# Performance work log

Measured on AMD Instinct MI355X. Metric: run time of the kernel, lower is better.

The kernel has to match this reference:

```python
import jax, jax.numpy as jnp
import numpy as np

VOCAB = 50257
EMBED = 256
OUT = 5
B = 512
S = 512

def setup_inputs() -> dict:
    key = jax.random.key(0)
    k1, k2, k3, k4, k5, k6 = jax.random.split(key, 6)
    input_x = jax.random.randint(k1, (B, S), 0, VOCAB, dtype=jnp.int64 if jax.config.jax_enable_x64 else jnp.int32)
    lengths = jax.random.randint(k2, (B,), 1, S + 1, dtype=jnp.int32)  # true ragged lengths in [1, S]
    input_y = jax.random.randint(k3, (B,), 0, OUT, dtype=jnp.int32)
    emb = jax.random.normal(k4, (VOCAB, EMBED), dtype=jnp.float32)
    W = jax.random.normal(k5, (OUT, EMBED), dtype=jnp.float32) * (1.0 / np.sqrt(EMBED))
    b = jax.random.normal(k6, (OUT,), dtype=jnp.float32) * 0.01
    return {"input_x": input_x, "lengths": lengths, "input_y": input_y, "emb": emb, "W": W, "b": b}

def reference(input_x, lengths, input_y, emb, W, b):
    # Embedding gather: [B, S, E]
    x = emb[input_x]
    # Ragged mean pooling via mask (replaces the per-sample Python loop)
    mask = (jnp.arange(S)[None, :] < lengths[:, None]).astype(x.dtype)  # [B, S]
    pooled = jnp.einsum('bse,bs->be', x, mask) / lengths[:, None].astype(x.dtype)  # [B, E]
    # Linear + log-softmax
    logits = pooled @ W.T + b  # [B, O]
    logp = jax.nn.log_softmax(logits, axis=-1)
    # NLLLoss (mean reduction)
    loss = -jnp.take_along_axis(logp, input_y[:, None].astype(jnp.int32), axis=1).mean()
    return loss
```

## Files before the change

kernel.cpp:

```cpp
#include <hip/hip_runtime.h>

#define VOCAB 50257
#define EMBED 256
#define OUT 5
#define BATCH 512
#define SEQ 512

__global__ __launch_bounds__(256) void k_embw(const float* __restrict__ emb,
                                              const float* __restrict__ W,
                                              float* __restrict__ embW) {
    __shared__ float sW[OUT * EMBED];
    for (int i = threadIdx.x; i < OUT * EMBED; i += 256) sW[i] = W[i];
    __syncthreads();

    const int wave = threadIdx.x >> 6;
    const int lane = threadIdx.x & 63;
    const int v = blockIdx.x * 4 + wave;
    if (v >= VOCAB) return;

    const float4 e = *(const float4*)(emb + (size_t)v * EMBED + lane * 4);

    float p[OUT];
#pragma unroll
    for (int o = 0; o < OUT; ++o) {
        const float4 w = *(const float4*)(sW + o * EMBED + lane * 4);
        p[o] = e.x * w.x + e.y * w.y + e.z * w.z + e.w * w.w;
    }

#pragma unroll
    for (int o = 0; o < OUT; ++o) {
        float val = p[o];
#pragma unroll
        for (int off = 32; off > 0; off >>= 1)
            val += __shfl_down(val, off, 64);
        if (lane == 0) embW[(size_t)v * OUT + o] = val;
    }
}

__global__ __launch_bounds__(256) void k_pool(const int* __restrict__ x,
                                              const int* __restrict__ lengths,
                                              const int* __restrict__ y,
                                              const float* __restrict__ bias,
                                              const float* __restrict__ embW,
                                              float* __restrict__ losses) {
    const int b = blockIdx.x;
    const int len = lengths[b];
    const int* xb = x + (size_t)b * SEQ;

    float acc[OUT] = {0.f, 0.f, 0.f, 0.f, 0.f};
    for (int s = threadIdx.x; s < len; s += 256) {
        const int tok = xb[s];
        const float* r = embW + (size_t)tok * OUT;
#pragma unroll
        for (int o = 0; o < OUT; ++o) acc[o] += r[o];
    }

#pragma unroll
    for (int o = 0; o < OUT; ++o) {
#pragma unroll
        for (int off = 32; off > 0; off >>= 1)
            acc[o] += __shfl_down(acc[o], off, 64);
    }

    __shared__ float red[4][OUT];
    const int wave = threadIdx.x >> 6;
    const int lane = threadIdx.x & 63;
    if (lane == 0) {
#pragma unroll
        for (int o = 0; o < OUT; ++o) red[wave][o] = acc[o];
    }
    __syncthreads();

    if (threadIdx.x == 0) {
        float logits[OUT];
        const float inv = 1.0f / (float)len;
#pragma unroll
        for (int o = 0; o < OUT; ++o)
            logits[o] = (red[0][o] + red[1][o] + red[2][o] + red[3][o]) * inv + bias[o];

        float m = logits[0];
#pragma unroll
        for (int o = 1; o < OUT; ++o) m = fmaxf(m, logits[o]);
        float sum = 0.f;
#pragma unroll
        for (int o = 0; o < OUT; ++o) sum += __expf(logits[o] - m);
        const float lse = m + __logf(sum);
        losses[b] = lse - logits[y[b]];
    }
}

__global__ __launch_bounds__(256) void k_reduce(const float* __restrict__ losses,
                                                float* __restrict__ out) {
    float v = losses[threadIdx.x] + losses[threadIdx.x + 256];
#pragma unroll
    for (int off = 32; off > 0; off >>= 1)
        v += __shfl_down(v, off, 64);
    __shared__ float red[4];
    if ((threadIdx.x & 63) == 0) red[threadIdx.x >> 6] = v;
    __syncthreads();
    if (threadIdx.x == 0)
        out[0] = (red[0] + red[1] + red[2] + red[3]) * (1.0f / (float)BATCH);
}

extern "C" void kernel_launch(void* const* d_in, const int* in_sizes, int n_in,
                              void* d_out, int out_size, void* d_ws, size_t ws_size,
                              hipStream_t stream) {
    const int*   x       = (const int*)d_in[0];
    const int*   lengths = (const int*)d_in[1];
    const int*   y       = (const int*)d_in[2];
    const float* emb     = (const float*)d_in[3];
    const float* W       = (const float*)d_in[4];
    const float* bias    = (const float*)d_in[5];

    float* embW   = (float*)d_ws;
    float* losses = embW + (size_t)VOCAB * OUT;

    k_embw<<<(VOCAB + 3) / 4, 256, 0, stream>>>(emb, W, embW);
    k_pool<<<BATCH, 256, 0, stream>>>(x, lengths, y, bias, embW, losses);
    k_reduce<<<1, 256, 0, stream>>>(losses, (float*)d_out);
}
```

Baseline: 114.1 us.

## Use grid-stride register-resident W projection, padded embW rows, and vectorized token loads

The vocab projection kernel becomes grid-stride over 1024 blocks. W is held in registers instead of shared memory, and each wave handles four vocab rows with 16-lane sub-reductions, so fewer shuffle steps are needed per row. The projected table is padded to 8 floats per row so the pooling kernel can gather with a float4 plus one scalar load, and tokens are read as int2 pairs with no loop. The change trades higher register pressure (80 floats of W per thread) for less shared-memory traffic, fewer blocks and fewer gather instructions, at the cost of a larger workspace.

```diff
diff --git a/kernel.cpp b/kernel.cpp
--- a/kernel.cpp
+++ b/kernel.cpp
@@ -5,35 +5,51 @@
 #define OUT 5
 #define BATCH 512
 #define SEQ 512
+#define PADO 8
 
 __global__ __launch_bounds__(256) void k_embw(const float* __restrict__ emb,
                                               const float* __restrict__ W,
                                               float* __restrict__ embW) {
-    __shared__ float sW[OUT * EMBED];
-    for (int i = threadIdx.x; i < OUT * EMBED; i += 256) sW[i] = W[i];
-    __syncthreads();
+    const int lane = threadIdx.x & 63;
+    const int sub  = lane >> 4;
+    const int col  = lane & 15;
 
-    const int wave = threadIdx.x >> 6;
-    const int lane = threadIdx.x & 63;
-    const int v = blockIdx.x * 4 + wave;
-    if (v >= VOCAB) return;
+    float4 w[OUT][4];
+#pragma unroll
+    for (int o = 0; o < OUT; ++o)
+#pragma unroll
+        for (int c = 0; c < 4; ++c)
+            w[o][c] = *(const float4*)(W + o * EMBED + col * 16 + c * 4);
 
-    const float4 e = *(const float4*)(emb + (size_t)v * EMBED + lane * 4);
+    const int waveId = (int)((blockIdx.x * 256u + threadIdx.x) >> 6);
+    const int nWaves = (int)gridDim.x * 4;
+    const int nQuad  = (VOCAB + 3) / 4;
 
-    float p[OUT];
+    for (int q = waveId; q < nQuad; q += nWaves) {
+        const int v = q * 4 + sub;
+        float p[OUT] = {0.f, 0.f, 0.f, 0.f, 0.f};
+        if (v < VOCAB) {
+            const float* row = emb + (size_t)v * EMBED + col * 16;
 #pragma unroll
-    for (int o = 0; o < OUT; ++o) {
-        const float4 w = *(const float4*)(sW + o * EMBED + lane * 4);
-        p[o] = e.x * w.x + e.y * w.y + e.z * w.z + e.w * w.w;
-    }
-
+            for (int c = 0; c < 4; ++c) {
+                const float4 e = *(const float4*)(row + c * 4);
 #pragma unroll
-    for (int o = 0; o < OUT; ++o) {
-        float val = p[o];
+                for (int o = 0; o < OUT; ++o)
+                    p[o] += e.x * w[o][c].x + e.y * w[o][c].y +
+                            e.z * w[o][c].z + e.w * w[o][c].w;
+            }
+        }
 #pragma unroll
-        for (int off = 32; off > 0; off >>= 1)
-            val += __shfl_down(val, off, 64);
-        if (lane == 0) embW[(size_t)v * OUT + o] = val;
+        for (int o = 0; o < OUT; ++o) {
+#pragma unroll
+            for (int off = 8; off > 0; off >>= 1)
+                p[o] += __shfl_down(p[o], off, 16);
+        }
+        if (col == 0 && v < VOCAB) {
+            float* dst = embW + (size_t)v * PADO;
+            *(float4*)dst = make_float4(p[0], p[1], p[2], p[3]);
+            dst[4] = p[4];
+        }
     }
 }
 
@@ -43,16 +59,24 @@
                                               const float* __restrict__ bias,
                                               const float* __restrict__ embW,
                                               float* __restrict__ losses) {
-    const int b = blockIdx.x;
+    const int b   = blockIdx.x;
     const int len = lengths[b];
-    const int* xb = x + (size_t)b * SEQ;
+    const int tid = threadIdx.x;
+
+    const int2 tk = ((const int2*)(x + (size_t)b * SEQ))[tid];
 
     float acc[OUT] = {0.f, 0.f, 0.f, 0.f, 0.f};
-    for (int s = threadIdx.x; s < len; s += 256) {
-        const int tok = xb[s];
-        const float* r = embW + (size_t)tok * OUT;
-#pragma unroll
-        for (int o = 0; o < OUT; ++o) acc[o] += r[o];
+    if (2 * tid < len) {
+        const float* r = embW + (size_t)tk.x * PADO;
+        const float4 a = *(const float4*)r;
+        const float a4 = r[4];
+        acc[0] += a.x; acc[1] += a.y; acc[2] += a.z; acc[3] += a.w; acc[4] += a4;
+    }
+    if (2 * tid + 1 < len) {
+        const float* r = embW + (size_t)tk.y * PADO;
+        const float4 a = *(const float4*)r;
+        const float a4 = r[4];
+        acc[0] += a.x; acc[1] += a.y; acc[2] += a.z; acc[3] += a.w; acc[4] += a4;
     }
 
 #pragma unroll
@@ -63,15 +87,15 @@
     }
 
     __shared__ float red[4][OUT];
-    const int wave = threadIdx.x >> 6;
-    const int lane = threadIdx.x & 63;
+    const int wave = tid >> 6;
+    const int lane = tid & 63;
     if (lane == 0) {
 #pragma unroll
         for (int o = 0; o < OUT; ++o) red[wave][o] = acc[o];
     }
     __syncthreads();
 
-    if (threadIdx.x == 0) {
+    if (tid == 0) {
         float logits[OUT];
         const float inv = 1.0f / (float)len;
 #pragma unroll
@@ -113,9 +137,9 @@
     const float* bias    = (const float*)d_in[5];
 
     float* embW   = (float*)d_ws;
-    float* losses = embW + (size_t)VOCAB * OUT;
+    float* losses = embW + (size_t)VOCAB * PADO;
 
-    k_embw<<<(VOCAB + 3) / 4, 256, 0, stream>>>(emb, W, embW);
+    k_embw<<<1024, 256, 0, stream>>>(emb, W, embW);
     k_pool<<<BATCH, 256, 0, stream>>>(x, lengths, y, bias, embW, losses);
     k_reduce<<<1, 256, 0, stream>>>(losses, (float*)d_out);
 }
```

After: 101.5 us. -11.1%, faster.

## Gather embedding rows directly per batch instead of precomputing vocab projection

Applied to the files above, without the earlier changes.

Drops the full-vocabulary emb·Wᵀ precompute, which read all 51 MB of the embedding table. Each batch row now gathers only its own token embeddings, pools them across 16 waves, projects the pooled vector with W, and adds its loss to the output atomically. The three kernels collapse into a memset plus one launch. Gathered traffic is about half the tokens times 1 KB each (~67 MB with duplicates), though the gathers may hit L2/MALL, and the atomic float sum makes the result order-dependent.

```diff
diff --git a/kernel.cpp b/kernel.cpp
--- a/kernel.cpp
+++ b/kernel.cpp
@@ -5,78 +5,63 @@
 #define OUT 5
 #define BATCH 512
 #define SEQ 512
+#define NT 1024
 
-__global__ __launch_bounds__(256) void k_embw(const float* __restrict__ emb,
-                                              const float* __restrict__ W,
-                                              float* __restrict__ embW) {
-    __shared__ float sW[OUT * EMBED];
-    for (int i = threadIdx.x; i < OUT * EMBED; i += 256) sW[i] = W[i];
+__global__ __launch_bounds__(NT) void k_direct(const int* __restrict__ x,
+                                               const int* __restrict__ lengths,
+                                               const int* __restrict__ y,
+                                               const float* __restrict__ emb,
+                                               const float* __restrict__ W,
+                                               const float* __restrict__ bias,
+                                               float* __restrict__ out) {
+    const int b    = blockIdx.x;
+    const int len  = lengths[b];
+    const int tid  = threadIdx.x;
+    const int wave = tid >> 6;
+    const int lane = tid & 63;
+
+    __shared__ int sx[SEQ];
+    if (tid < SEQ) sx[tid] = x[(size_t)b * SEQ + tid];
     __syncthreads();
 
-    const int wave = threadIdx.x >> 6;
-    const int lane = threadIdx.x & 63;
-    const int v = blockIdx.x * 4 + wave;
-    if (v >= VOCAB) return;
+    float4 acc = make_float4(0.f, 0.f, 0.f, 0.f);
+#pragma unroll 4
+    for (int s = wave; s < len; s += 16) {
+        const float4 r = ((const float4*)(emb + (size_t)sx[s] * EMBED))[lane];
+        acc.x += r.x; acc.y += r.y; acc.z += r.z; acc.w += r.w;
+    }
 
-    const float4 e = *(const float4*)(emb + (size_t)v * EMBED + lane * 4);
+    __shared__ float4 sS[NT];
+    sS[tid] = acc;
+    __syncthreads();
+
+    if (wave != 0) return;
+
+    float4 S = sS[lane];
+#pragma unroll
+    for (int w = 1; w < 16; ++w) {
+        const float4 t = sS[w * 64 + lane];
+        S.x += t.x; S.y += t.y; S.z += t.z; S.w += t.w;
+    }
 
     float p[OUT];
 #pragma unroll
     for (int o = 0; o < OUT; ++o) {
-        const float4 w = *(const float4*)(sW + o * EMBED + lane * 4);
-        p[o] = e.x * w.x + e.y * w.y + e.z * w.z + e.w * w.w;
+        const float4 w4 = ((const float4*)(W + o * EMBED))[lane];
+        p[o] = S.x * w4.x + S.y * w4.y + S.z * w4.z + S.w * w4.w;
     }
-
-#pragma unroll
-    for (int o = 0; o < OUT; ++o) {
-        float val = p[o];
-#pragma unroll
-        for (int off = 32; off > 0; off >>= 1)
-            val += __shfl_down(val, off, 64);
-        if (lane == 0) embW[(size_t)v * OUT + o] = val;
-    }
-}
-
-__global__ __launch_bounds__(256) void k_pool(const int* __restrict__ x,
-                                              const int* __restrict__ lengths,
-                                              const int* __restrict__ y,
-                                              const float* __restrict__ bias,
-                                              const float* __restrict__ embW,
-                                              float* __restrict__ losses) {
-    const int b = blockIdx.x;
-    const int len = lengths[b];
-    const int* xb = x + (size_t)b * SEQ;
-
-    float acc[OUT] = {0.f, 0.f, 0.f, 0.f, 0.f};
-    for (int s = threadIdx.x; s < len; s += 256) {
-        const int tok = xb[s];
-        const float* r = embW + (size_t)tok * OUT;
-#pragma unroll
-        for (int o = 0; o < OUT; ++o) acc[o] += r[o];
-    }
-
 #pragma unroll
     for (int o = 0; o < OUT; ++o) {
 #pragma unroll
         for (int off = 32; off > 0; off >>= 1)
-            acc[o] += __shfl_down(acc[o], off, 64);
+            p[o] += __shfl_down(p[o], off, 64);
     }
 
-    __shared__ float red[4][OUT];
-    const int wave = threadIdx.x >> 6;
-    const int lane = threadIdx.x & 63;
     if (lane == 0) {
+        const float inv = 1.0f / (float)len;
+        float logits[OUT];
 #pragma unroll
-        for (int o = 0; o < OUT; ++o) red[wave][o] = acc[o];
-    }
-    __syncthreads();
-
-    if (threadIdx.x == 0) {
-        float logits[OUT];
-        const float inv = 1.0f / (float)len;
-#pragma unroll
-        for (int o = 0; o < OUT; ++o)
-            logits[o] = (red[0][o] + red[1][o] + red[2][o] + red[3][o]) * inv + bias[o];
+        for (int o = 0; o < OUT; ++o) logits[o] = p[o] * inv + bias[o];
 
         float m = logits[0];
 #pragma unroll
@@ -85,21 +70,10 @@
 #pragma unroll
         for (int o = 0; o < OUT; ++o) sum += __expf(logits[o] - m);
         const float lse = m + __logf(sum);
-        losses[b] = lse - logits[y[b]];
+        const float loss = lse - logits[y[b]];
+
+        atomicAdd(out, loss * (1.0f / (float)BATCH));
     }
-}
-
-__global__ __launch_bounds__(256) void k_reduce(const float* __restrict__ losses,
-                                                float* __restrict__ out) {
-    float v = losses[threadIdx.x] + losses[threadIdx.x + 256];
-#pragma unroll
-    for (int off = 32; off > 0; off >>= 1)
-        v += __shfl_down(v, off, 64);
-    __shared__ float red[4];
-    if ((threadIdx.x & 63) == 0) red[threadIdx.x >> 6] = v;
-    __syncthreads();
-    if (threadIdx.x == 0)
-        out[0] = (red[0] + red[1] + red[2] + red[3]) * (1.0f / (float)BATCH);
 }
 
 extern "C" void kernel_launch(void* const* d_in, const int* in_sizes, int n_in,
@@ -112,10 +86,7 @@
     const float* W       = (const float*)d_in[4];
     const float* bias    = (const float*)d_in[5];
 
-    float* embW   = (float*)d_ws;
-    float* losses = embW + (size_t)VOCAB * OUT;
-
-    k_embw<<<(VOCAB + 3) / 4, 256, 0, stream>>>(emb, W, embW);
-    k_pool<<<BATCH, 256, 0, stream>>>(x, lengths, y, bias, embW, losses);
-    k_reduce<<<1, 256, 0, stream>>>(losses, (float*)d_out);
+    hipMemsetAsync(d_out, 0, sizeof(float), stream);
+    k_direct<<<BATCH, NT, 0, stream>>>(x, lengths, y, emb, W, bias,
+                                       (float*)d_out);
 }
```

Result: faster. 106.6 us (-6.5%).
